# Optimization experiments

Measured on AMD Instinct MI355X. Metric: run time of the kernel, lower is better.

## Reference

```python
import jax, jax.numpy as jnp
import numpy as np

# Standard SMPL kinematic tree parents (kintree_table)
PARENTS = np.array([-1, 0, 0, 0, 1, 2, 3, 4, 5, 6, 7, 8, 9, 9, 9,
                    12, 13, 14, 16, 17, 18, 19, 20, 21])
NV, NJ, NB, NP = 6890, 24, 10, 207


def rodrigues(r):
    """Axis-angle [N,3] -> rotation matrices [N,3,3] (Rodrigues formula)."""
    theta = jnp.linalg.norm(r, axis=1, keepdims=True) + 1e-8  # [N,1]
    rh = r / theta                                            # [N,3]
    cos = jnp.cos(theta)[..., None]                           # [N,1,1]
    sin = jnp.sin(theta)[..., None]
    z = jnp.zeros_like(rh[:, 0])
    m = jnp.stack([z, -rh[:, 2], rh[:, 1],
                   rh[:, 2], z, -rh[:, 0],
                   -rh[:, 1], rh[:, 0], z], axis=1).reshape(-1, 3, 3)
    dot = rh[:, :, None] * rh[:, None, :]                     # outer product
    eye = jnp.eye(3, dtype=r.dtype)
    return cos * eye + (1.0 - cos) * dot + sin * m


def setup_inputs() -> dict:
    key = jax.random.key(0)
    ks = jax.random.split(key, 9)
    B = 512
    betas = jax.random.normal(ks[0], (B, NB), dtype=jnp.float32)
    thetas = jax.random.normal(ks[1], (B, NJ * 3), dtype=jnp.float32) * 0.3
    trans = jax.random.normal(ks[2], (B, 3), dtype=jnp.float32)
    scale = jnp.ones((1,), dtype=jnp.float32)
    v_template = jax.random.normal(ks[3], (NV, 3), dtype=jnp.float32)
    shapedirs = jax.random.normal(ks[4], (NV, 3, NB), dtype=jnp.float32) * 0.01
    posedirs = jax.random.normal(ks[5], (NV, 3, NP), dtype=jnp.float32) * 0.01
    Jr = jax.random.uniform(ks[6], (NJ, NV), dtype=jnp.float32)
    J_regressor = Jr / jnp.sum(Jr, axis=1, keepdims=True)
    w = jax.random.uniform(ks[7], (NV, NJ), dtype=jnp.float32)
    weights = w / jnp.sum(w, axis=1, keepdims=True)
    return {"betas": betas, "thetas": thetas, "trans": trans, "scale": scale,
            "v_template": v_template, "shapedirs": shapedirs,
            "posedirs": posedirs, "J_regressor": J_regressor,
            "weights": weights}


def reference(betas, thetas, trans, scale, v_template, shapedirs, posedirs,
              J_regressor, weights):
    B = betas.shape[0]
    dt = betas.dtype
    # Shape blend shapes: v_shaped [B, 6890, 3]
    v_shaped = jnp.einsum('bs,vcs->bvc', betas, shapedirs) + v_template
    # Rest-pose joints J(beta): [B, 24, 3]
    J = jnp.einsum('jv,bvc->bjc', J_regressor, v_shaped)
    # Local rotations from axis-angle, root scaled by `scale`
    lRs = rodrigues(thetas.reshape(-1, 3)).reshape(B, NJ, 3, 3)
    lRs = lRs.at[:, 0].multiply(scale[0])
    # Local joint offsets: root keeps J[:,0], children use J[i] - J[parent[i]]
    parents = jnp.asarray(PARENTS)
    t = J - J[:, jnp.clip(parents, 0)]
    t = t.at[:, 0].set(J[:, 0])
    # Local 4x4 transforms [B, 24, 4, 4]
    top = jnp.concatenate([lRs, t[..., None]], axis=3)          # [B,24,3,4]
    bottom = jnp.broadcast_to(jnp.array([0., 0., 0., 1.], dtype=dt),
                              (B, NJ, 1, 4))
    A = jnp.concatenate([top, bottom], axis=2)
    # Kinematic chain accumulation (fixed 24-joint tree)
    results = [A[:, 0]]
    for i in range(1, NJ):
        results.append(results[PARENTS[i]] @ A[:, i])
    stacked = jnp.stack(results, axis=1)                         # [B,24,4,4]
    # Remove rest-pose joint locations from translation column
    Jh = jnp.concatenate([J, jnp.zeros((B, NJ, 1), dtype=dt)], axis=2)
    deformed = jnp.einsum('bjxy,bjy->bjx', stacked, Jh)          # [B,24,4]
    G = stacked.at[..., 3].add(-deformed)
    # Pose blend shapes from non-root rotations
    lrotmin = (lRs[:, 1:] - jnp.eye(3, dtype=dt)).reshape(B, -1)  # [B,207]
    v_posed = v_shaped + jnp.einsum('bp,vcp->bvc', lrotmin, posedirs)
    # Linear blend skinning
    T = jnp.einsum('bjxy,vj->bvxy', G, weights)                  # [B,6890,4,4]
    vh = jnp.concatenate([v_posed, jnp.ones((B, NV, 1), dtype=dt)], axis=2)
    v = jnp.einsum('bvxy,bvy->bvx', T, vh)[:, :, :3]
    result = v + trans[:, None, :]
    joints = jnp.einsum('jv,bvc->bjc', J_regressor, result)
    return result, joints
```

## Files before the change

kernel.cpp:

```cpp
#include <hip/hip_runtime.h>

#define NVERT 6890
#define NJNT  24
#define NBETA 10
#define NPOSE 207
#define NBATCH 512
#define KPAD 224
#define MROWS 20736
#define NVC (NVERT * 3)

typedef __attribute__((ext_vector_type(8))) short short8;
typedef __attribute__((ext_vector_type(4))) float floatx4;

__constant__ int c_par[NJNT]   = {-1,0,0,0,1,2,3,4,5,6,7,8,9,9,9,12,13,14,16,17,18,19,20,21};
__constant__ int c_depth[NJNT] = { 0,1,1,1,2,2,2,3,3,3,4,4,4,4,4,5,5,5,6,6,7,7,8,8};

static __device__ __forceinline__ unsigned short f2bf(float x) {
  union { float f; unsigned u; } v; v.f = x;
  unsigned r = (v.u + 0x7FFFu + ((v.u >> 16) & 1u)) >> 16;
  return (unsigned short)r;
}
static __device__ __forceinline__ float bf2f(unsigned short h) {
  union { unsigned u; float f; } v; v.u = (unsigned)h << 16;
  return v.f;
}

__global__ __launch_bounds__(256) void k_buildA(
    const float* __restrict__ pdir, const float* __restrict__ sd,
    const float* __restrict__ vt, unsigned short* __restrict__ AT) {
  const int idx = blockIdx.x * 256 + threadIdx.x;
  const int kk = idx & 31;
  const int row = (idx >> 5) % MROWS;
  const int kt = idx / (MROWS * 32);
  const int k = kt * 32 + kk;
  float val = 0.f;
  if (row < NVC) {
    if (k < NPOSE)            val = pdir[(size_t)row * NPOSE + k];
    else if (k < NPOSE + 10)  val = sd[(size_t)row * 10 + (k - NPOSE)];
    else if (k == NPOSE + 10) val = vt[row];
  }
  AT[idx] = f2bf(val);
}

__global__ __launch_bounds__(256) void k_buildW(
    const float* __restrict__ wgt, unsigned short* __restrict__ W16) {
  const int idx = blockIdx.x * 256 + threadIdx.x;
  const int v = idx >> 6, c = idx & 63, j = c & 31, h = c >> 5;
  const float w = (v < NVERT && j < 24) ? wgt[(size_t)v * 24 + j] : 0.f;
  const unsigned short hi = f2bf(w);
  W16[idx] = h ? f2bf(w - bf2f(hi)) : hi;
}

__global__ __launch_bounds__(256) void k_jreg1(
    const float* __restrict__ Jr, const float* __restrict__ vt,
    const float* __restrict__ sd, float* __restrict__ wsJP) {
  const int jc = blockIdx.x, j = jc / 3, c = jc % 3;
  const int v0 = blockIdx.y * 864;
  const int vend = min(NVERT, v0 + 864);
  const int tid = threadIdx.x;
  float acc[11];
  #pragma unroll
  for (int k = 0; k < 11; ++k) acc[k] = 0.f;
  for (int v = v0 + tid; v < vend; v += 256) {
    const float w = Jr[j * NVERT + v];
    acc[0] += w * vt[v * 3 + c];
    const float* s = sd + (size_t)v * 30 + c * 10;
    #pragma unroll
    for (int k = 0; k < 10; ++k) acc[1 + k] += w * s[k];
  }
  #pragma unroll
  for (int off = 32; off > 0; off >>= 1) {
    #pragma unroll
    for (int k = 0; k < 11; ++k) acc[k] += __shfl_down(acc[k], off, 64);
  }
  __shared__ float red[4][11];
  const int lane = tid & 63, wv = tid >> 6;
  if (lane == 0) {
    #pragma unroll
    for (int k = 0; k < 11; ++k) red[wv][k] = acc[k];
  }
  __syncthreads();
  if (tid == 0) {
    #pragma unroll
    for (int k = 0; k < 11; ++k)
      wsJP[(size_t)(blockIdx.y * 72 + jc) * 11 + k] =
          red[0][k] + red[1][k] + red[2][k] + red[3][k];
  }
}

__global__ __launch_bounds__(256, 2) void k_chain3(
    const float* __restrict__ betas, const float* __restrict__ thetas,
    const float* __restrict__ scale, const float* __restrict__ trans,
    const float* __restrict__ wsJP,
    unsigned short* __restrict__ BT, unsigned short* __restrict__ G16) {
  __shared__ __align__(16) float sJ[792];
  __shared__ __align__(16) float sJJ[4][72];
  __shared__ __align__(16) float sM[4][288];
  __shared__ __align__(16) unsigned short sG[4][1024];
  __shared__ __align__(16) unsigned short sB[4][KPAD];

  const int tid = threadIdx.x;
  const int wv = tid >> 6, lane = tid & 63;
  const int b = blockIdx.x * 4 + wv;

  if (tid < 72) {
    #pragma unroll
    for (int k = 0; k < 11; ++k) {
      float s = 0.f;
      #pragma unroll
      for (int c8 = 0; c8 < 8; ++c8) s += wsJP[(size_t)(c8 * 72 + tid) * 11 + k];
      if (k == 0) sJ[tid] = s;
      else        sJ[72 + tid * 10 + (k - 1)] = s;
    }
  }
  #pragma unroll
  for (int r = 0; r < 4; ++r) {
    sG[wv][lane * 16 + r * 4 + 0] = 0; sG[wv][lane * 16 + r * 4 + 1] = 0;
    sG[wv][lane * 16 + r * 4 + 2] = 0; sG[wv][lane * 16 + r * 4 + 3] = 0;
  }
  __syncthreads();

  float R[9], t[3], M[12], Jx = 0.f, Jy = 0.f, Jz = 0.f;
  const int i = lane;
  if (i < NJNT) {
    #pragma unroll
    for (int c = 0; c < 3; ++c) {
      float a = sJ[i * 3 + c];
      const float* d = sJ + 72 + (i * 3 + c) * 10;
      #pragma unroll
      for (int s = 0; s < NBETA; ++s) a += d[s] * betas[b * NBETA + s];
      if (c == 0) Jx = a; else if (c == 1) Jy = a; else Jz = a;
    }
    sJJ[wv][i * 3 + 0] = Jx; sJJ[wv][i * 3 + 1] = Jy; sJJ[wv][i * 3 + 2] = Jz;
    const float rx = thetas[b * 72 + i * 3 + 0];
    const float ry = thetas[b * 72 + i * 3 + 1];
    const float rz = thetas[b * 72 + i * 3 + 2];
    const float th = sqrtf(rx * rx + ry * ry + rz * rz) + 1e-8f;
    const float inv = 1.f / th;
    const float x = rx * inv, y = ry * inv, z = rz * inv;
    const float cs = cosf(th), sn = sinf(th), omc = 1.f - cs;
    R[0] = cs + omc * x * x;     R[1] = omc * x * y - sn * z; R[2] = omc * x * z + sn * y;
    R[3] = omc * x * y + sn * z; R[4] = cs + omc * y * y;     R[5] = omc * y * z - sn * x;
    R[6] = omc * x * z - sn * y; R[7] = omc * y * z + sn * x; R[8] = cs + omc * z * z;
    if (i == 0) {
      const float sc = scale[0];
      #pragma unroll
      for (int k = 0; k < 9; ++k) R[k] *= sc;
    } else {
      #pragma unroll
      for (int k = 0; k < 9; ++k)
        sB[wv][(i - 1) * 9 + k] = f2bf(R[k] - ((k == 0 || k == 4 || k == 8) ? 1.f : 0.f));
    }
  }
  if (i == 0) {
    #pragma unroll
    for (int s = 0; s < NBETA; ++s) sB[wv][NPOSE + s] = f2bf(betas[b * NBETA + s]);
    sB[wv][NPOSE + 10] = 0x3F80;
    #pragma unroll
    for (int k = NPOSE + 11; k < KPAD; ++k) sB[wv][k] = 0;
  }
  __syncthreads();

  if (i < NJNT) {
    if (i == 0) { t[0] = Jx; t[1] = Jy; t[2] = Jz; }
    else {
      const int p = c_par[i];
      t[0] = Jx - sJJ[wv][p * 3 + 0];
      t[1] = Jy - sJJ[wv][p * 3 + 1];
      t[2] = Jz - sJJ[wv][p * 3 + 2];
    }
    if (i == 0) {
      #pragma unroll
      for (int r = 0; r < 3; ++r) {
        M[r*4+0] = R[r*3+0]; M[r*4+1] = R[r*3+1]; M[r*4+2] = R[r*3+2]; M[r*4+3] = t[r];
      }
      #pragma unroll
      for (int k = 0; k < 12; ++k) sM[wv][k] = M[k];
    }
  }
  __syncthreads();

  for (int lvl = 1; lvl <= 8; ++lvl) {
    if (i < NJNT && c_depth[i] == lvl) {
      const float* Mp = sM[wv] + c_par[i] * 12;
      #pragma unroll
      for (int r = 0; r < 3; ++r) {
        const float p0 = Mp[r*4+0], p1 = Mp[r*4+1], p2 = Mp[r*4+2], p3 = Mp[r*4+3];
        M[r*4+0] = p0*R[0] + p1*R[3] + p2*R[6];
        M[r*4+1] = p0*R[1] + p1*R[4] + p2*R[7];
        M[r*4+2] = p0*R[2] + p1*R[5] + p2*R[8];
        M[r*4+3] = p0*t[0] + p1*t[1] + p2*t[2] + p3;
      }
      #pragma unroll
      for (int k = 0; k < 12; ++k) sM[wv][i * 12 + k] = M[k];
    }
    __syncthreads();
  }

  if (i < NJNT) {
    #pragma unroll
    for (int r = 0; r < 3; ++r) {
      M[r*4+3] = M[r*4+3] - (M[r*4+0]*Jx + M[r*4+1]*Jy + M[r*4+2]*Jz)
               + trans[b * 3 + r];
    }
    #pragma unroll
    for (int e = 0; e < 12; ++e) {
      const float g = M[e];
      const unsigned short hi = f2bf(g);
      sG[wv][e * 32 + i]       = hi;
      sG[wv][512 + e * 32 + i] = f2bf(g - bf2f(hi));
    }
  }
  __syncthreads();

  *(uint4*)(G16 + (size_t)b * 1024 + lane * 16)     = *(uint4*)&sG[wv][lane * 16];
  *(uint4*)(G16 + (size_t)b * 1024 + lane * 16 + 8) = *(uint4*)&sG[wv][lane * 16 + 8];
  if (lane < 28)
    *(uint4*)(BT + ((size_t)(lane >> 2) * NBATCH + b) * 32 + (lane & 3) * 8) =
        *(uint4*)&sB[wv][lane * 8];
}

__global__ __launch_bounds__(256, 3) void k_skin4(
    const unsigned short* __restrict__ AT, const unsigned short* __restrict__ BT,
    const unsigned short* __restrict__ W16, const unsigned short* __restrict__ G16,
    float* __restrict__ out) {
  __shared__ __align__(16) char smem[33536];
  unsigned short* sAs = (unsigned short*)smem;
  unsigned short* sBs = (unsigned short*)(smem + 15360);
  float* sV           = (float*)smem;
  unsigned short* sG2 = (unsigned short*)(smem + 13056);

  const int tid = threadIdx.x;
  const int wv = tid >> 6, lane = tid & 63;
  const int q = lane >> 4, n = lane & 15;

  const int fb = blockIdx.x;
  const int vb = (fb & 7) * 108 + (fb >> 3);
  const int b0 = (vb & 7) * 64;
  const int by = vb >> 3;
  const int vc0 = by * 192;

  floatx4 acc[3][4];
  #pragma unroll
  for (int mt = 0; mt < 3; ++mt)
    #pragma unroll
    for (int nt = 0; nt < 4; ++nt) acc[mt][nt] = (floatx4)(0.f);

  const int srow = tid >> 2, sj = tid & 3;

  for (int kt = 0; kt < 7; ++kt) {
    if (kt) __syncthreads();
    #pragma unroll
    for (int it = 0; it < 3; ++it)
      *(uint4*)(sAs + (it * 64 + srow) * 40 + sj * 8) =
          *(const uint4*)(AT + ((size_t)kt * MROWS + vc0 + it * 64 + srow) * 32 + sj * 8);
    *(uint4*)(sBs + srow * 40 + sj * 8) =
        *(const uint4*)(BT + ((size_t)kt * NBATCH + b0 + srow) * 32 + sj * 8);
    __syncthreads();
    short8 af[3], bfr[4];
    #pragma unroll
    for (int mt = 0; mt < 3; ++mt)
      af[mt] = *(const short8*)(sAs + (48 * wv + 16 * mt + n) * 40 + q * 8);
    #pragma unroll
    for (int nt = 0; nt < 4; ++nt)
      bfr[nt] = *(const short8*)(sBs + (16 * nt + n) * 40 + q * 8);
    #pragma unroll
    for (int mt = 0; mt < 3; ++mt)
      #pragma unroll
      for (int nt = 0; nt < 4; ++nt)
        acc[mt][nt] = __builtin_amdgcn_mfma_f32_16x16x32_bf16(
            af[mt], bfr[nt], acc[mt][nt], 0, 0, 0);
  }

  short8 wh[4], wl[4];
  #pragma unroll
  for (int vt = 0; vt < 4; ++vt) {
    const unsigned short* wr = W16 + (size_t)(by * 64 + vt * 16 + n) * 64;
    wh[vt] = *(const short8*)(wr + q * 8);
    wl[vt] = *(const short8*)(wr + 32 + q * 8);
  }

  for (int nt = 0; nt < 4; ++nt) {
    for (int s = 0; s < 2; ++s) {
      __syncthreads();
      if (s == 0) {
        #pragma unroll
        for (int mt = 0; mt < 3; ++mt)
          #pragma unroll
          for (int r = 0; r < 4; ++r)
            sV[(48 * wv + 16 * mt + 4 * q + r) * 17 + n] = acc[mt][nt][r];
      }
      const int bg0 = b0 + nt * 16 + s * 8;
      for (int i = tid; i < 1024; i += 256) {
        const int row = i >> 2, c4 = i & 3;
        const int t = row >> 5, rem = row & 31;
        *(uint4*)(sG2 + row * 40 + c4 * 8) =
            *(const uint4*)(G16 + (size_t)(bg0 + t) * 1024 + rem * 32 + c4 * 8);
      }
      __syncthreads();
      #pragma unroll
      for (int bb = 0; bb < 2; ++bb) {
        const int t = wv * 2 + bb;
        const int col = s * 8 + t;
        const int bg = b0 + nt * 16 + col;
        const short8 gh = *(const short8*)(sG2 + (t * 32 + n) * 40 + q * 8);
        const short8 gl = *(const short8*)(sG2 + (t * 32 + 16 + n) * 40 + q * 8);
        #pragma unroll
        for (int vt = 0; vt < 4; ++vt) {
          floatx4 a2 = (floatx4)(0.f);
          a2 = __builtin_amdgcn_mfma_f32_16x16x32_bf16(gh, wl[vt], a2, 0, 0, 0);
          a2 = __builtin_amdgcn_mfma_f32_16x16x32_bf16(gl, wh[vt], a2, 0, 0, 0);
          a2 = __builtin_amdgcn_mfma_f32_16x16x32_bf16(gh, wh[vt], a2, 0, 0, 0);
          const float X = sV[(48 * vt + 3 * n + 0) * 17 + col];
          const float Y = sV[(48 * vt + 3 * n + 1) * 17 + col];
          const float Z = sV[(48 * vt + 3 * n + 2) * 17 + col];
          const float o = a2[0] * X + a2[1] * Y + a2[2] * Z + a2[3];
          const int vc = vc0 + 48 * vt + 3 * n + q;
          if (q < 3 && vc < NVC)
            out[(size_t)bg * NVC + vc] = o;
        }
      }
    }
  }
}

__global__ __launch_bounds__(256) void k_joints(
    const float* __restrict__ Jr, const float* __restrict__ res,
    float* __restrict__ joints) {
  const int b = blockIdx.x;
  const int lane = threadIdx.x & 63, wv = threadIdx.x >> 6;
  float acc[18];
  #pragma unroll
  for (int k = 0; k < 18; ++k) acc[k] = 0.f;
  const float* rb = res + (size_t)b * NVC;
  for (int v = lane; v < NVERT; v += 64) {
    const float r0 = rb[v*3+0], r1 = rb[v*3+1], r2 = rb[v*3+2];
    #pragma unroll
    for (int k = 0; k < 6; ++k) {
      const int j = wv + 4 * k;
      const float w = Jr[j * NVERT + v];
      acc[k*3+0] += w * r0; acc[k*3+1] += w * r1; acc[k*3+2] += w * r2;
    }
  }
  #pragma unroll
  for (int off = 32; off > 0; off >>= 1) {
    #pragma unroll
    for (int k = 0; k < 18; ++k) acc[k] += __shfl_down(acc[k], off, 64);
  }
  if (lane == 0) {
    #pragma unroll
    for (int k = 0; k < 6; ++k) {
      const int j = wv + 4 * k;
      joints[(size_t)b * 72 + j * 3 + 0] = acc[k*3+0];
      joints[(size_t)b * 72 + j * 3 + 1] = acc[k*3+1];
      joints[(size_t)b * 72 + j * 3 + 2] = acc[k*3+2];
    }
  }
}

extern "C" void kernel_launch(void* const* d_in, const int* in_sizes, int n_in,
                              void* d_out, int out_size, void* d_ws, size_t ws_size,
                              hipStream_t stream) {
  const float* betas  = (const float*)d_in[0];
  const float* thetas = (const float*)d_in[1];
  const float* trans  = (const float*)d_in[2];
  const float* scale  = (const float*)d_in[3];
  const float* vtpl   = (const float*)d_in[4];
  const float* sd     = (const float*)d_in[5];
  const float* pdir   = (const float*)d_in[6];
  const float* Jr     = (const float*)d_in[7];
  const float* wgt    = (const float*)d_in[8];
  float* out = (float*)d_out;

  float* ws   = (float*)d_ws;
  float* wsJP = ws;
  unsigned short* AT  = (unsigned short*)(ws + 6336);
  unsigned short* BT  = AT + (size_t)MROWS * KPAD;
  unsigned short* W16 = BT + (size_t)NBATCH * KPAD;
  unsigned short* G16 = W16 + (size_t)6912 * 64;

  k_buildA<<<(MROWS * KPAD) / 256, 256, 0, stream>>>(pdir, sd, vtpl, AT);
  k_buildW<<<(6912 * 64) / 256, 256, 0, stream>>>(wgt, W16);
  k_jreg1<<<dim3(72, 8), 256, 0, stream>>>(Jr, vtpl, sd, wsJP);
  k_chain3<<<NBATCH / 4, 256, 0, stream>>>(betas, thetas, scale, trans, wsJP, BT, G16);
  k_skin4<<<864, 256, 0, stream>>>(AT, BT, W16, G16, out);
  k_joints<<<NBATCH, 256, 0, stream>>>(Jr, out, out + (size_t)NBATCH * NVC);
}
```

Before: 186.6 us.

## Split joint regression across vertex chunks and batch pairs with two-stage reduction

The joint-regression kernel is split into eight vertex chunks per batch, and each block handles two batches so every J_regressor load is reused twice. Partial sums go to a workspace that reuses the AT buffer, and a second small kernel adds the eight partials. This raises parallelism from 512 long-running blocks to 2048 shorter ones and halves regressor traffic per result. In exchange it adds a kernel launch, and the 36 accumulators raise register pressure.

```diff
diff --git a/kernel.cpp b/kernel.cpp
--- a/kernel.cpp
+++ b/kernel.cpp
@@ -324,38 +324,56 @@
   }
 }
 
-__global__ __launch_bounds__(256) void k_joints(
+__global__ __launch_bounds__(256) void k_jnt1(
     const float* __restrict__ Jr, const float* __restrict__ res,
-    float* __restrict__ joints) {
-  const int b = blockIdx.x;
+    float* __restrict__ wsJ2) {
+  const int b0 = blockIdx.x * 2;
+  const int chunk = blockIdx.y;
+  const int v0 = chunk * 864;
+  const int vend = min(NVERT, v0 + 864);
   const int lane = threadIdx.x & 63, wv = threadIdx.x >> 6;
-  float acc[18];
-  #pragma unroll
-  for (int k = 0; k < 18; ++k) acc[k] = 0.f;
-  const float* rb = res + (size_t)b * NVC;
-  for (int v = lane; v < NVERT; v += 64) {
-    const float r0 = rb[v*3+0], r1 = rb[v*3+1], r2 = rb[v*3+2];
+  float acc[36];
+  #pragma unroll
+  for (int k = 0; k < 36; ++k) acc[k] = 0.f;
+  const float* rA = res + (size_t)b0 * NVC;
+  const float* rB = res + (size_t)(b0 + 1) * NVC;
+  for (int v = v0 + lane; v < vend; v += 64) {
+    const float a0 = rA[v * 3 + 0], a1 = rA[v * 3 + 1], a2 = rA[v * 3 + 2];
+    const float e0 = rB[v * 3 + 0], e1 = rB[v * 3 + 1], e2 = rB[v * 3 + 2];
     #pragma unroll
     for (int k = 0; k < 6; ++k) {
       const int j = wv + 4 * k;
       const float w = Jr[j * NVERT + v];
-      acc[k*3+0] += w * r0; acc[k*3+1] += w * r1; acc[k*3+2] += w * r2;
+      acc[k*6+0] += w * a0; acc[k*6+1] += w * a1; acc[k*6+2] += w * a2;
+      acc[k*6+3] += w * e0; acc[k*6+4] += w * e1; acc[k*6+5] += w * e2;
     }
   }
   #pragma unroll
   for (int off = 32; off > 0; off >>= 1) {
     #pragma unroll
-    for (int k = 0; k < 18; ++k) acc[k] += __shfl_down(acc[k], off, 64);
+    for (int k = 0; k < 36; ++k) acc[k] += __shfl_down(acc[k], off, 64);
   }
   if (lane == 0) {
     #pragma unroll
     for (int k = 0; k < 6; ++k) {
       const int j = wv + 4 * k;
-      joints[(size_t)b * 72 + j * 3 + 0] = acc[k*3+0];
-      joints[(size_t)b * 72 + j * 3 + 1] = acc[k*3+1];
-      joints[(size_t)b * 72 + j * 3 + 2] = acc[k*3+2];
-    }
-  }
+      float* d0 = wsJ2 + ((size_t)b0 * 8 + chunk) * 72 + j * 3;
+      d0[0] = acc[k*6+0]; d0[1] = acc[k*6+1]; d0[2] = acc[k*6+2];
+      float* d1 = wsJ2 + ((size_t)(b0 + 1) * 8 + chunk) * 72 + j * 3;
+      d1[0] = acc[k*6+3]; d1[1] = acc[k*6+4]; d1[2] = acc[k*6+5];
+    }
+  }
+}
+
+__global__ __launch_bounds__(256) void k_jnt2(
+    const float* __restrict__ wsJ2, float* __restrict__ joints) {
+  const int idx = blockIdx.x * 256 + threadIdx.x;
+  const int b = idx / 72, jc = idx - b * 72;
+  float s = 0.f;
+  #pragma unroll
+  for (int c8 = 0; c8 < 8; ++c8)
+    s += wsJ2[((size_t)b * 8 + c8) * 72 + jc];
+  joints[idx] = s;
 }
 
 extern "C" void kernel_launch(void* const* d_in, const int* in_sizes, int n_in,
@@ -378,11 +396,13 @@
   unsigned short* BT  = AT + (size_t)MROWS * KPAD;
   unsigned short* W16 = BT + (size_t)NBATCH * KPAD;
   unsigned short* G16 = W16 + (size_t)6912 * 64;
+  float* wsJ2 = (float*)AT;
 
   k_buildA<<<(MROWS * KPAD) / 256, 256, 0, stream>>>(pdir, sd, vtpl, AT);
   k_buildW<<<(6912 * 64) / 256, 256, 0, stream>>>(wgt, W16);
   k_jreg1<<<dim3(72, 8), 256, 0, stream>>>(Jr, vtpl, sd, wsJP);
   k_chain3<<<NBATCH / 4, 256, 0, stream>>>(betas, thetas, scale, trans, wsJP, BT, G16);
   k_skin4<<<864, 256, 0, stream>>>(AT, BT, W16, G16, out);
-  k_joints<<<NBATCH, 256, 0, stream>>>(Jr, out, out + (size_t)NBATCH * NVC);
-}
+  k_jnt1<<<dim3(NBATCH / 2, 8), 256, 0, stream>>>(Jr, out, wsJ2);
+  k_jnt2<<<(NBATCH * 72) / 256, 256, 0, stream>>>(wsJ2, out + (size_t)NBATCH * NVC);
+}
```

Measured after the change: 171.5 us (median of 2 runs). 1.09x faster.
